# Performance work log

Hardware: AMD Instinct MI355X
Metric: run time of the kernel (lower is better)

The kernel has to match this reference:

```python
import jax, jax.numpy as jnp
import numpy as np

N, P, S, ENT = 256, 4, 40, 60
E = 1 + P + S + ENT          # 105 graph nodes (query + paras + sents + ents)
D = 1024                     # input_dim == hidden_dim
H, T = 8, 3                  # gnn heads, edge types
DH = D // H                  # per-head output dim
NEG = -1e30


def setup_inputs() -> dict:
    key = jax.random.key(0)
    ks = jax.random.split(key, 12)
    f = lambda k, sh, s: jax.random.normal(k, sh, jnp.float32) * s
    return {
        "query_vec": f(ks[0], (N, D), 1.0),
        "para_state": f(ks[1], (N, P, D), 1.0),
        "sent_state": f(ks[2], (N, S, D), 1.0),
        "ent_state": f(ks[3], (N, ENT, D), 1.0),
        "para_mask": jax.random.randint(ks[4], (N, P), 0, 2).astype(jnp.float32),
        "sent_mask": jax.random.randint(ks[5], (N, S), 0, 2).astype(jnp.float32),
        "ent_mask": jax.random.randint(ks[6], (N, ENT), 0, 2).astype(jnp.float32),
        "adj": jax.random.randint(ks[7], (N, E, E), 0, T + 1).astype(jnp.int32),
        "W": f(ks[8], (H, T, D, DH), 0.05),        # per head/edge-type projection
        "a": f(ks[9], (H, T, 2 * DH), 0.05),       # GAT attention vector [a1;a2]
        "qW1": f(ks[10], (H, T, D, 2 * DH), 0.05), # query-gate layer 1
        "qW2": f(ks[11], (H, T, 2 * DH, 2 * DH), 0.05),  # query-gate layer 2
    }


def _graph_block(x, query_vec, node_mask, adj, W, a, qW1, qW2):
    # x: [N,E,D], node_mask: [N,E,1], adj: [N,E,E] int (0 = no edge, 1..T = edge type)
    # per head/edge-type projections: [H,T,N,E,DH]
    h = jnp.einsum('ned,htdk->htnek', x, W)
    # query-conditioned gate (q_attn=True): sigmoid(relu(q @ W1) @ W2) -> [H,T,N,2DH]
    g = jax.nn.sigmoid(jnp.einsum('htnk,htkm->htnm',
                                  jax.nn.relu(jnp.einsum('nd,htdk->htnk', query_vec, qW1)),
                                  qW2))
    # decomposed GAT score: score[i,j] = lrelu((g1*h_i)@a1 + (g2*h_j)@a2)
    a1, a2 = a[..., :DH], a[..., DH:]
    f1 = jnp.einsum('htnek,htnk->htne', h, g[..., :DH] * a1[:, :, None, :])
    f2 = jnp.einsum('htnek,htnk->htne', h, g[..., DH:] * a2[:, :, None, :])
    score = jax.nn.leaky_relu(f1[..., :, None] + f2[..., None, :], 0.2)  # [H,T,N,E,E]
    # accumulate only where adj matches the edge type (i+1)
    etype = (jnp.arange(T, dtype=adj.dtype) + 1)[None, :, None, None, None]
    scores = jnp.sum(jnp.where(adj[None, None] == etype, score, 0.0), axis=1)  # [H,N,E,E]
    scores = jnp.where(adj[None] > 0, scores, NEG)
    coefs = jax.nn.softmax(scores, axis=-1)                 # [H,N,E,E]
    # original uses the last edge-type projection, node-masked, for aggregation
    h_last = h[:, -1] * node_mask[None]                     # [H,N,E,DH]
    out = jnp.einsum('hnij,hnjd->hnid', coefs, h_last)      # [H,N,E,DH]
    out = jnp.transpose(out, (1, 2, 0, 3)).reshape(x.shape[0], E, H * DH)
    out = jax.nn.relu(out)                                  # dropout p=0 in eval
    return out + x                                          # residual (identity align)


def reference(query_vec, para_state, sent_state, ent_state,
              para_mask, sent_mask, ent_mask, adj, W, a, qW1, qW2):
    x = jnp.concatenate([query_vec[:, None, :], para_state, sent_state, ent_state], axis=1)  # [N,E,D]
    node_mask = jnp.concatenate(
        [jnp.ones((x.shape[0], 1), x.dtype), para_mask, sent_mask, ent_mask], axis=-1)[..., None]  # [N,E,1]
    graph_state = _graph_block(x, query_vec, node_mask, adj, W, a, qW1, qW2)  # [N,E,D]
    return graph_state
```

## Files before the change

### kernel.cpp

```cpp
#include <hip/hip_runtime.h>
#include <stdint.h>


typedef unsigned short u16;
typedef __bf16 bf16;
typedef __bf16 bf16x8 __attribute__((ext_vector_type(8)));
typedef float f32x4 __attribute__((ext_vector_type(4)));

#define N_ 256
#define E_ 105
#define D_ 1024
#define H_ 8
#define DH_ 128
#define NE_ 26880

__device__ __forceinline__ u16 f2b(float f) { bf16 h = (bf16)f; return __builtin_bit_cast(u16, h); }
__device__ __forceinline__ float b2f(u16 u) { bf16 h = __builtin_bit_cast(bf16, u); return (float)h; }

#define AS1 __attribute__((address_space(1)))
#define AS3 __attribute__((address_space(3)))

__device__ __forceinline__ void load16_lds(const void* g, void* l) {
  __builtin_amdgcn_global_load_lds((AS1 void*)(unsigned long long)(uintptr_t)g,
                                   (AS3 void*)l, 16, 0, 0);
}

__device__ __forceinline__ void gemm128(u16* lds, const u16* A, const u16* B, int K,
                                        int lda, int ldb, f32x4 (&acc)[4][4]) {
  u16* lA = lds;
  u16* lB = lds + 8192;
  const int tid  = threadIdx.x;
  const int lane = tid & 63;
  const int wave = tid >> 6;
  const int ln15 = lane & 15;
  const int lq   = lane >> 4;
  const int wRow = (wave >> 1) * 64;
  const int wCol = (wave & 1) * 64;

  const int iters = K >> 6;
  for (int kt = 0; kt < iters; ++kt) {
    const char* Ab = (const char*)A + kt * 128;
    const char* Bb = (const char*)B + kt * 128;
#pragma unroll
    for (int m = 0; m < 4; ++m) {
      int ci  = m * 256 + tid;
      int row = ci >> 3;
      int g   = (ci & 7) ^ (row & 7);
      char* dstA = (char*)lA + m * 4096 + wave * 1024;
      char* dstB = (char*)lB + m * 4096 + wave * 1024;
      load16_lds(Ab + (long)row * ((long)lda * 2) + g * 16, dstA);
      load16_lds(Bb + (long)row * ((long)ldb * 2) + g * 16, dstB);
    }
    __syncthreads();
#pragma unroll
    for (int ks = 0; ks < 2; ++ks) {
      const int cc = ks * 4 + lq;
      bf16x8 af[4], bfv[4];
#pragma unroll
      for (int i = 0; i < 4; ++i) {
        int r = wRow + i * 16 + ln15;
        af[i] = *(const bf16x8*)&lA[r * 64 + ((cc ^ (r & 7)) << 3)];
        int c = wCol + i * 16 + ln15;
        bfv[i] = *(const bf16x8*)&lB[c * 64 + ((cc ^ (c & 7)) << 3)];
      }
#pragma unroll
      for (int i = 0; i < 4; ++i)
#pragma unroll
        for (int j = 0; j < 4; ++j)
          acc[i][j] = __builtin_amdgcn_mfma_f32_16x16x32_bf16(af[i], bfv[j], acc[i][j], 0, 0, 0);
    }
    __syncthreads();
  }
}

__device__ __forceinline__ void zero_acc(f32x4 (&acc)[4][4]) {
  f32x4 z = {0.f, 0.f, 0.f, 0.f};
#pragma unroll
  for (int i = 0; i < 4; ++i)
#pragma unroll
    for (int j = 0; j < 4; ++j) acc[i][j] = z;
}

__global__ __launch_bounds__(256) void k_cast(const float* src, u16* dst, long n) {
  long i = ((long)blockIdx.x * 256 + threadIdx.x) * 4;
  if (i >= n) return;
  float4 v = *(const float4*)(src + i);
  ushort4 o;
  o.x = f2b(v.x); o.y = f2b(v.y); o.z = f2b(v.z); o.w = f2b(v.w);
  *(ushort4*)(dst + i) = o;
}

__global__ __launch_bounds__(256) void k_build(const float* q, const float* para,
                                               const float* sent, const float* ent,
                                               const float* pm, const float* sm,
                                               const float* em, u16* x, float* nmask) {
  long idx = (long)blockIdx.x * 256 + threadIdx.x;
  if (idx >= (long)NE_ * 128) return;
  int ne = (int)(idx >> 7), dc = (int)(idx & 127);
  int n = ne / E_, e = ne - n * E_;
  const float* src;
  if (e == 0)      src = q + (long)n * D_;
  else if (e < 5)  src = para + (long)(n * 4 + (e - 1)) * D_;
  else if (e < 45) src = sent + (long)(n * 40 + (e - 5)) * D_;
  else             src = ent + (long)(n * 60 + (e - 45)) * D_;
  float4 v0 = *(const float4*)(src + dc * 8);
  float4 v1 = *(const float4*)(src + dc * 8 + 4);
  uint4 o;
  o.x = (unsigned)f2b(v0.x) | ((unsigned)f2b(v0.y) << 16);
  o.y = (unsigned)f2b(v0.z) | ((unsigned)f2b(v0.w) << 16);
  o.z = (unsigned)f2b(v1.x) | ((unsigned)f2b(v1.y) << 16);
  o.w = (unsigned)f2b(v1.z) | ((unsigned)f2b(v1.w) << 16);
  *(uint4*)(x + (long)ne * D_ + dc * 8) = o;
  if (dc == 0) {
    float mv;
    if (e == 0)      mv = 1.f;
    else if (e < 5)  mv = pm[n * 4 + e - 1];
    else if (e < 45) mv = sm[n * 40 + e - 5];
    else             mv = em[n * 60 + e - 45];
    nmask[ne] = mv;
  }
}

__global__ __launch_bounds__(256) void k_tr(const float* src, u16* dst, int R, int C,
                                            long sStr, long dStr) {
  __shared__ u16 t[32][33];
  const int bz = blockIdx.y;
  const int tilesC = C >> 5;
  const int tr = (blockIdx.x / tilesC) << 5;
  const int tc = (blockIdx.x % tilesC) << 5;
  const int lr = threadIdx.x >> 5;
  const int lc = threadIdx.x & 31;
#pragma unroll
  for (int i = 0; i < 4; ++i)
    t[lr + i * 8][lc] = f2b(src[bz * sStr + (long)(tr + lr + i * 8) * C + tc + lc]);
  __syncthreads();
#pragma unroll
  for (int i = 0; i < 4; ++i)
    dst[bz * dStr + (long)(tc + lr + i * 8) * R + tr + lc] = t[lc][lr + i * 8];
}

__global__ __launch_bounds__(256) void k_qw1(const u16* x, const u16* qW1t, u16* r_bf) {
  __shared__ u16 shm[16384];
  const int bx = blockIdx.x;
  const int ht = bx >> 2, nt = (bx >> 1) & 1, mt = bx & 1;
  f32x4 acc[4][4];
  zero_acc(acc);
  gemm128(shm, x + (long)nt * 128 * (E_ * D_), qW1t + ((long)ht * 256 + mt * 128) * D_,
          1024, E_ * D_, 1024, acc);
  const int tid = threadIdx.x, lane = tid & 63, wave = tid >> 6;
  const int ln15 = lane & 15, lq = lane >> 4;
  const int wRow = (wave >> 1) * 64, wCol = (wave & 1) * 64;
#pragma unroll
  for (int rt = 0; rt < 4; ++rt)
#pragma unroll
    for (int ct = 0; ct < 4; ++ct)
#pragma unroll
      for (int rg = 0; rg < 4; ++rg) {
        int n = nt * 128 + wRow + rt * 16 + lq * 4 + rg;
        int m = mt * 128 + wCol + ct * 16 + ln15;
        float v = acc[rt][ct][rg];
        if (v < 0.f) v = 0.f;
        r_bf[((long)ht * 256 + n) * 256 + m] = f2b(v);
      }
}

__global__ __launch_bounds__(256) void k_qw2(const u16* r_bf, const u16* qW2t, const float* a,
                                             u16* ga) {
  __shared__ u16 shm[16384];
  const int bx = blockIdx.x;
  const int ht = bx >> 2, nt = (bx >> 1) & 1, mt = bx & 1;
  f32x4 acc[4][4];
  zero_acc(acc);
  gemm128(shm, r_bf + ((long)ht * 256 + nt * 128) * 256, qW2t + ((long)ht * 256 + mt * 128) * 256,
          256, 256, 256, acc);
  const int tid = threadIdx.x, lane = tid & 63, wave = tid >> 6;
  const int ln15 = lane & 15, lq = lane >> 4;
  const int wRow = (wave >> 1) * 64, wCol = (wave & 1) * 64;
#pragma unroll
  for (int rt = 0; rt < 4; ++rt)
#pragma unroll
    for (int ct = 0; ct < 4; ++ct)
#pragma unroll
      for (int rg = 0; rg < 4; ++rg) {
        int n = nt * 128 + wRow + rt * 16 + lq * 4 + rg;
        int m = mt * 128 + wCol + ct * 16 + ln15;
        float v = acc[rt][ct][rg];
        float sig = 1.f / (1.f + __expf(-v));
        float gv = sig * a[ht * 256 + m];
        int s = m >> 7, kk = m & 127;
        ga[(((long)ht * 2 + s) * 256 + n) * 128 + kk] = f2b(gv);
      }
}

__global__ __launch_bounds__(256) void k_w12(const u16* ga, const u16* Wb, u16* w12) {
  __shared__ u16 shm[16384];
  const int bx = blockIdx.x;
  const int c = bx >> 4, r2 = bx & 15;
  const int nt = r2 >> 3, dt = r2 & 7;
  const int ht = c >> 1;
  f32x4 acc[4][4];
  zero_acc(acc);
  gemm128(shm, ga + ((long)c * 256 + nt * 128) * 128, Wb + (long)ht * 131072 + dt * 128 * 128,
          128, 128, 128, acc);
  const int tid = threadIdx.x, lane = tid & 63, wave = tid >> 6;
  const int ln15 = lane & 15, lq = lane >> 4;
  const int wRow = (wave >> 1) * 64, wCol = (wave & 1) * 64;
#pragma unroll
  for (int rt = 0; rt < 4; ++rt)
#pragma unroll
    for (int ct = 0; ct < 4; ++ct)
#pragma unroll
      for (int rg = 0; rg < 4; ++rg) {
        int n = nt * 128 + wRow + rt * 16 + lq * 4 + rg;
        int d = dt * 128 + wCol + ct * 16 + ln15;
        w12[((long)n * 48 + c) * 1024 + d] = f2b(acc[rt][ct][rg]);
      }
}

__global__ __launch_bounds__(256) void k_f(const u16* x, const u16* w12, float* F) {
  __shared__ u16 shm[16384];
  const int n = blockIdx.x;
  f32x4 acc[4][4];
  zero_acc(acc);
  gemm128(shm, x + (long)n * E_ * D_, w12 + (long)n * 48 * 1024, 1024, 1024, 1024, acc);
  const int tid = threadIdx.x, lane = tid & 63, wave = tid >> 6;
  const int ln15 = lane & 15, lq = lane >> 4;
  const int wRow = (wave >> 1) * 64, wCol = (wave & 1) * 64;
#pragma unroll
  for (int rt = 0; rt < 4; ++rt)
#pragma unroll
    for (int ct = 0; ct < 4; ++ct)
#pragma unroll
      for (int rg = 0; rg < 4; ++rg) {
        int e = wRow + rt * 16 + lq * 4 + rg;
        int c = wCol + ct * 16 + ln15;
        if (e < 105 && c < 48) F[((long)n * 48 + c) * 105 + e] = acc[rt][ct][rg];
      }
}

__global__ __launch_bounds__(256) void k_h(const u16* x, const u16* Wt, const float* nmask,
                                           float* out) {
  __shared__ u16 shm[16384];
  const int bx = blockIdx.x;
  const int h = bx / 210;
  const int ne0 = (bx % 210) * 128;
  f32x4 acc[4][4];
  zero_acc(acc);
  gemm128(shm, x + (long)ne0 * D_, Wt + (long)h * DH_ * D_, 1024, 1024, 1024, acc);
  const int tid = threadIdx.x, lane = tid & 63, wave = tid >> 6;
  const int ln15 = lane & 15, lq = lane >> 4;
  const int wRow = (wave >> 1) * 64, wCol = (wave & 1) * 64;
#pragma unroll
  for (int rt = 0; rt < 4; ++rt)
#pragma unroll
    for (int ct = 0; ct < 4; ++ct)
#pragma unroll
      for (int rg = 0; rg < 4; ++rg) {
        int nel = wRow + rt * 16 + lq * 4 + rg;
        int k   = wCol + ct * 16 + ln15;
        shm[k * 128 + (nel ^ ((k & 15) << 3))] = f2b(acc[rt][ct][rg]);
      }
  __syncthreads();
  char* ob = (char*)out;
  for (int it = tid; it < 16384; it += 256) {
    int k = it >> 7, nel = it & 127;
    int ne = ne0 + nel;
    int n = ne / 105;
    int j = ne - n * 105;
    int t = k * 224 + j * 2;
    long gb = ((long)(n * 105 + (t >> 9)) << 12) + ((long)h << 9) + (t & 511);
    u16 v = shm[k * 128 + (nel ^ ((k & 15) << 3))];
    float mv = nmask[ne];
    *(u16*)(ob + gb) = (mv != 0.f) ? v : (u16)0;
    if (j == 104) {
#pragma unroll
      for (int p = 1; p <= 7; ++p) {
        int tp = t + p * 2;
        long gp = ((long)(n * 105 + (tp >> 9)) << 12) + ((long)h << 9) + (tp & 511);
        *(u16*)(ob + gp) = 0;
      }
    }
  }
}

__global__ __launch_bounds__(256) void k_attn(const float* F, const int* adj, const u16* x,
                                              float* out) {
  const int h = blockIdx.x >> 8;
  const int n = blockIdx.x & 255;
  __shared__ u16 cb[112 * 128];
  __shared__ float f1s[3][112];
  __shared__ float f2s[3][112];
  const int tid = threadIdx.x;
  const int lane = tid & 63, wave = tid >> 6;

  for (int i = tid; i < 630; i += 256) {
    int t = i / 210;
    int rm = i - t * 210;
    int s = rm / 105;
    int e = rm - s * 105;
    float v = F[((long)n * 48 + (h * 3 + t) * 2 + s) * 105 + e];
    if (s == 0) f1s[t][e] = v; else f2s[t][e] = v;
  }
  {
    unsigned* cbz = (unsigned*)cb;
    for (int i = tid; i < 112 * 64; i += 256) cbz[i] = 0;
  }
  __syncthreads();

  {
    const int* abase = adj + (long)n * (E_ * E_);
    const int j1 = 64 + lane;
    const bool j1v = lane < 41;
    float f20a = f2s[0][lane], f20b = f2s[1][lane], f20c = f2s[2][lane];
    float f21a = 0.f, f21b = 0.f, f21c = 0.f;
    if (j1v) { f21a = f2s[0][j1]; f21b = f2s[1][j1]; f21c = f2s[2][j1]; }
    int i = wave;
    int av0 = abase[i * E_ + lane];
    int av1 = j1v ? abase[i * E_ + j1] : 0;
    while (i < 105) {
      const int inext = i + 4;
      int bv0 = 0, bv1 = 0;
      if (inext < 105) {
        bv0 = abase[inext * E_ + lane];
        bv1 = j1v ? abase[inext * E_ + j1] : 0;
      }
      float f11 = f1s[0][i], f12 = f1s[1][i], f13 = f1s[2][i];
      float s0, s1;
      {
        float f1v = (av0 == 1) ? f11 : ((av0 == 2) ? f12 : f13);
        float f2v = (av0 == 1) ? f20a : ((av0 == 2) ? f20b : f20c);
        float s = f1v + f2v;
        s = (s < 0.f) ? 0.2f * s : s;
        s0 = (av0 > 0) ? s : -1e30f;
      }
      {
        float f1v = (av1 == 1) ? f11 : ((av1 == 2) ? f12 : f13);
        float f2v = (av1 == 1) ? f21a : ((av1 == 2) ? f21b : f21c);
        float s = f1v + f2v;
        s = (s < 0.f) ? 0.2f * s : s;
        s1 = (av1 > 0) ? s : -1e30f;
      }
      float m = fmaxf(s0, s1);
#pragma unroll
      for (int d = 1; d < 64; d <<= 1) m = fmaxf(m, __shfl_xor(m, d));
      float e0 = __expf(s0 - m);
      float e1 = j1v ? __expf(s1 - m) : 0.f;
      float sum = e0 + e1;
#pragma unroll
      for (int d = 1; d < 64; d <<= 1) sum += __shfl_xor(sum, d);
      float inv = 1.f / sum;
      const int rsw = i & 15;
      cb[i * 128 + ((((lane >> 3) ^ rsw) << 3) + (lane & 7))] = f2b(e0 * inv);
      if (j1v)
        cb[i * 128 + ((((j1 >> 3) ^ rsw) << 3) + (lane & 7))] = f2b(e1 * inv);
      av0 = bv0; av1 = bv1;
      i = inext;
    }
  }
  __syncthreads();

  const char* hb = (const char*)out + (((long)n * 105) << 12) + ((long)h << 9);
  const int ln15 = lane & 15, lq = lane >> 4;
  const int nmt = (wave < 3) ? 2 : 1;
  f32x4 acc[2][8];
  {
    f32x4 z = {0.f, 0.f, 0.f, 0.f};
#pragma unroll
    for (int a_ = 0; a_ < 2; ++a_)
#pragma unroll
      for (int b_ = 0; b_ < 8; ++b_) acc[a_][b_] = z;
  }
#pragma unroll
  for (int ks = 0; ks < 4; ++ks) {
    const int cc = ks * 4 + lq;
    const int ccb = (cc < 14) ? cc : 0;
    bf16x8 bfr[8];
#pragma unroll
    for (int jn = 0; jn < 8; ++jn) {
      int k = jn * 16 + ln15;
      int t = k * 224 + ccb * 16;
      bfr[jn] = *(const bf16x8*)(hb + ((long)(t >> 9) << 12) + (t & 511));
    }
#pragma unroll
    for (int im = 0; im < 2; ++im) {
      if (im < nmt) {
        int i = (wave + im * 4) * 16 + ln15;
        bf16x8 af = *(const bf16x8*)&cb[i * 128 + ((cc ^ (i & 15)) << 3)];
#pragma unroll
        for (int jn = 0; jn < 8; ++jn)
          acc[im][jn] = __builtin_amdgcn_mfma_f32_16x16x32_bf16(af, bfr[jn], acc[im][jn], 0, 0, 0);
      }
    }
  }
  __syncthreads();
  for (int im = 0; im < nmt; ++im)
    for (int jn = 0; jn < 8; ++jn)
#pragma unroll
      for (int rg = 0; rg < 4; ++rg) {
        int i = (wave + im * 4) * 16 + lq * 4 + rg;
        if (i < 105) {
          int k = jn * 16 + ln15;
          long off = ((long)(n * E_ + i)) * D_ + h * DH_ + k;
          float v = acc[im][jn][rg];
          v = v < 0.f ? 0.f : v;
          out[off] = v + b2f(x[off]);
        }
      }
}

extern "C" void kernel_launch(void* const* d_in, const int* in_sizes, int n_in,
                              void* d_out, int out_size, void* d_ws, size_t ws_size,
                              hipStream_t stream) {
  const float* q    = (const float*)d_in[0];
  const float* para = (const float*)d_in[1];
  const float* sent = (const float*)d_in[2];
  const float* ent  = (const float*)d_in[3];
  const float* pm   = (const float*)d_in[4];
  const float* sm   = (const float*)d_in[5];
  const float* em   = (const float*)d_in[6];
  const int*   adj  = (const int*)d_in[7];
  const float* W    = (const float*)d_in[8];
  const float* a    = (const float*)d_in[9];
  const float* qW1  = (const float*)d_in[10];
  const float* qW2  = (const float*)d_in[11];
  float* out = (float*)d_out;
  char* ws = (char*)d_ws;

  u16*   x     = (u16*)(ws);
  float* nmask = (float*)(ws + 55050240);
  u16*   Wb    = (u16*)(ws + 55682048);
  u16*   Wt    = (u16*)(ws + 61973504);
  u16*   qW1t  = (u16*)(ws + 64070656);
  u16*   qW2t  = (u16*)(ws + 76653568);
  u16*   r_bf  = (u16*)(ws + 79799296);
  u16*   ga    = (u16*)(ws + 82945024);
  u16*   w12   = (u16*)(ws + 86090752);
  float* F     = (float*)(ws + 111420416);

  k_build<<<13440, 256, 0, stream>>>(q, para, sent, ent, pm, sm, em, x, nmask);
  k_cast<<<3072, 256, 0, stream>>>(W, Wb, 3145728);
  k_tr<<<dim3(256, 24), 256, 0, stream>>>(qW1, qW1t, 1024, 256, 262144, 262144);
  k_tr<<<dim3(64, 24), 256, 0, stream>>>(qW2, qW2t, 256, 256, 65536, 65536);
  k_tr<<<dim3(128, 8), 256, 0, stream>>>(W + 262144, Wt, 1024, 128, 393216, 131072);
  k_qw1<<<96, 256, 0, stream>>>(x, qW1t, r_bf);
  k_qw2<<<96, 256, 0, stream>>>(r_bf, qW2t, a, ga);
  k_w12<<<768, 256, 0, stream>>>(ga, Wb, w12);
  k_f<<<256, 256, 0, stream>>>(x, w12, F);
  k_h<<<1680, 256, 0, stream>>>(x, Wt, nmask, out);
  k_attn<<<2048, 256, 0, stream>>>(F, adj, x, out);
}
```

Baseline: 707.8 us.

## Restructure softmax into 16-lane row groups and stage epilogue through LDS for vector stores

The softmax phase now gives each 16-lane group of a wave its own attention row, so a wave handles four rows per iteration. Each lane covers seven columns and the reductions need only four shuffle steps instead of six; the prefetch of the next row's adjacency is dropped. The epilogue writes the ReLU'd MFMA accumulators into LDS in two row passes and then reads them back as float4, adding the bf16 residual from 4-wide loads. This turns scattered scalar global stores into coalesced 16-byte stores, at the cost of extra LDS traffic and barriers.

After: 661.0 us. 6.6% less time.

```diff
diff --git a/kernel.cpp b/kernel.cpp
--- a/kernel.cpp
+++ b/kernel.cpp
@@ -309,52 +309,62 @@
 
   {
     const int* abase = adj + (long)n * (E_ * E_);
-    const int j1 = 64 + lane;
-    const bool j1v = lane < 41;
-    float f20a = f2s[0][lane], f20b = f2s[1][lane], f20c = f2s[2][lane];
-    float f21a = 0.f, f21b = 0.f, f21c = 0.f;
-    if (j1v) { f21a = f2s[0][j1]; f21b = f2s[1][j1]; f21c = f2s[2][j1]; }
-    int i = wave;
-    int av0 = abase[i * E_ + lane];
-    int av1 = j1v ? abase[i * E_ + j1] : 0;
-    while (i < 105) {
-      const int inext = i + 4;
-      int bv0 = 0, bv1 = 0;
-      if (inext < 105) {
-        bv0 = abase[inext * E_ + lane];
-        bv1 = j1v ? abase[inext * E_ + j1] : 0;
-      }
-      float f11 = f1s[0][i], f12 = f1s[1][i], f13 = f1s[2][i];
-      float s0, s1;
-      {
-        float f1v = (av0 == 1) ? f11 : ((av0 == 2) ? f12 : f13);
-        float f2v = (av0 == 1) ? f20a : ((av0 == 2) ? f20b : f20c);
-        float s = f1v + f2v;
-        s = (s < 0.f) ? 0.2f * s : s;
-        s0 = (av0 > 0) ? s : -1e30f;
-      }
-      {
-        float f1v = (av1 == 1) ? f11 : ((av1 == 2) ? f12 : f13);
-        float f2v = (av1 == 1) ? f21a : ((av1 == 2) ? f21b : f21c);
-        float s = f1v + f2v;
-        s = (s < 0.f) ? 0.2f * s : s;
-        s1 = (av1 > 0) ? s : -1e30f;
-      }
-      float m = fmaxf(s0, s1);
-#pragma unroll
-      for (int d = 1; d < 64; d <<= 1) m = fmaxf(m, __shfl_xor(m, d));
-      float e0 = __expf(s0 - m);
-      float e1 = j1v ? __expf(s1 - m) : 0.f;
-      float sum = e0 + e1;
-#pragma unroll
-      for (int d = 1; d < 64; d <<= 1) sum += __shfl_xor(sum, d);
+    const int g  = lane >> 4;
+    const int lg = lane & 15;
+    float f2r[3][7];
+#pragma unroll
+    for (int m = 0; m < 7; ++m) {
+      int j = lg + m * 16;
+      bool jv = j < 105;
+#pragma unroll
+      for (int t = 0; t < 3; ++t) f2r[t][m] = jv ? f2s[t][j] : 0.f;
+    }
+    for (int it = 0; it < 7; ++it) {
+      int i = it * 16 + wave * 4 + g;
+      bool iv = i < 105;
+      int ir = iv ? i : 0;
+      int av[7];
+#pragma unroll
+      for (int m = 0; m < 7; ++m) {
+        int j = lg + m * 16;
+        av[m] = (iv && j < 105) ? abase[ir * E_ + j] : 0;
+      }
+      float f11 = f1s[0][ir], f12 = f1s[1][ir], f13 = f1s[2][ir];
+      float s[7];
+#pragma unroll
+      for (int m = 0; m < 7; ++m) {
+        int a_ = av[m];
+        float f1v = (a_ == 1) ? f11 : ((a_ == 2) ? f12 : f13);
+        float f2v = (a_ == 1) ? f2r[0][m] : ((a_ == 2) ? f2r[1][m] : f2r[2][m]);
+        float sv = f1v + f2v;
+        sv = (sv < 0.f) ? 0.2f * sv : sv;
+        s[m] = (a_ > 0) ? sv : -1e30f;
+      }
+      float mm = s[0];
+#pragma unroll
+      for (int m = 1; m < 7; ++m) mm = fmaxf(mm, s[m]);
+#pragma unroll
+      for (int d = 1; d < 16; d <<= 1) mm = fmaxf(mm, __shfl_xor(mm, d));
+      float e[7];
+      float sum = 0.f;
+#pragma unroll
+      for (int m = 0; m < 7; ++m) {
+        int j = lg + m * 16;
+        e[m] = (j < 105) ? __expf(s[m] - mm) : 0.f;
+        sum += e[m];
+      }
+#pragma unroll
+      for (int d = 1; d < 16; d <<= 1) sum += __shfl_xor(sum, d);
       float inv = 1.f / sum;
-      const int rsw = i & 15;
-      cb[i * 128 + ((((lane >> 3) ^ rsw) << 3) + (lane & 7))] = f2b(e0 * inv);
-      if (j1v)
-        cb[i * 128 + ((((j1 >> 3) ^ rsw) << 3) + (lane & 7))] = f2b(e1 * inv);
-      av0 = bv0; av1 = bv1;
-      i = inext;
+      if (iv) {
+        const int rsw = i & 15;
+#pragma unroll
+        for (int m = 0; m < 7; ++m) {
+          int j = lg + m * 16;
+          if (j < 105)
+            cb[i * 128 + ((((j >> 3) ^ rsw) << 3) + (j & 7))] = f2b(e[m] * inv);
+        }
+      }
     }
   }
   __syncthreads();
@@ -393,19 +403,36 @@
     }
   }
   __syncthreads();
-  for (int im = 0; im < nmt; ++im)
-    for (int jn = 0; jn < 8; ++jn)
-#pragma unroll
-      for (int rg = 0; rg < 4; ++rg) {
-        int i = (wave + im * 4) * 16 + lq * 4 + rg;
-        if (i < 105) {
-          int k = jn * 16 + ln15;
-          long off = ((long)(n * E_ + i)) * D_ + h * DH_ + k;
-          float v = acc[im][jn][rg];
-          v = v < 0.f ? 0.f : v;
-          out[off] = v + b2f(x[off]);
+
+  float* sf = (float*)cb;
+#pragma unroll
+  for (int pass = 0; pass < 2; ++pass) {
+    const int rbase = pass * 54;
+    const int rcnt  = pass ? 51 : 54;
+    for (int im = 0; im < nmt; ++im)
+#pragma unroll
+      for (int jn = 0; jn < 8; ++jn)
+#pragma unroll
+        for (int rg = 0; rg < 4; ++rg) {
+          int i = (wave + im * 4) * 16 + lq * 4 + rg;
+          if (i >= rbase && i < rbase + rcnt && i < 105) {
+            int k = jn * 16 + ln15;
+            float v = acc[im][jn][rg];
+            sf[(i - rbase) * 132 + k] = v < 0.f ? 0.f : v;
+          }
         }
-      }
+    __syncthreads();
+    for (int c = tid; c < rcnt * 32; c += 256) {
+      int r = c >> 5, k4 = (c & 31) << 2;
+      int i = rbase + r;
+      float4 v = *(const float4*)&sf[r * 132 + k4];
+      long xb = ((long)(n * E_ + i)) * D_ + h * DH_ + k4;
+      ushort4 xv = *(const ushort4*)&x[xb];
+      v.x += b2f(xv.x); v.y += b2f(xv.y); v.z += b2f(xv.z); v.w += b2f(xv.w);
+      *(float4*)&out[xb] = v;
+    }
+    if (pass == 0) __syncthreads();
+  }
 }
 
 extern "C" void kernel_launch(void* const* d_in, const int* in_sizes, int n_in,
```
